# Kernel tuning notes

Measured on AMD Instinct MI355X. Metric: run time of the kernel, lower is better.

Reference implementation:

```python
import jax, jax.numpy as jnp
import numpy as np

N = 100000
E = 3200000
D = 128


def setup_inputs() -> dict:
    key = jax.random.key(0)
    k1, k2, k3, k4 = jax.random.split(key, 4)
    x = jax.random.normal(k1, (N, D), dtype=jnp.float32)
    edge_index = jax.random.randint(k2, (2, E), 0, N, dtype=jnp.int64)
    W1 = jax.random.normal(k3, (D, 16), dtype=jnp.float32) * (1.0 / np.sqrt(D))
    b1 = jnp.zeros((16,), dtype=jnp.float32)
    W2 = jax.random.normal(k4, (16, 2), dtype=jnp.float32) * (1.0 / np.sqrt(16))
    b2 = jnp.zeros((2,), dtype=jnp.float32)
    return {"x": x, "edge_index": edge_index, "W1": W1, "b1": b1, "W2": W2, "b2": b2}


def _gcn_conv(h, src, dst, norm, W, b):
    # transform first (out_dim <= in_dim), then normalized scatter-add aggregation
    h = h @ W                                   # [N, out]
    msg = h[src] * norm[:, None]                # [E+N, out] gathered messages
    agg = jax.ops.segment_sum(msg, dst, num_segments=N)
    return agg + b


def reference(x, edge_index, W1, b1, W2, b2):
    loops = jnp.arange(N, dtype=edge_index.dtype)
    src = jnp.concatenate([edge_index[0], loops])   # row (message source)
    dst = jnp.concatenate([edge_index[1], loops])   # col (aggregation target)
    # symmetric GCN normalization: deg over dst, norm = d^-1/2[src] * d^-1/2[dst]
    deg = jax.ops.segment_sum(jnp.ones_like(src, dtype=x.dtype), dst, num_segments=N)
    dinv = jnp.where(deg > 0, jax.lax.rsqrt(deg), 0.0)
    norm = dinv[src] * dinv[dst]

    h = _gcn_conv(x, src, dst, norm, W1, b1)
    h = jax.nn.relu(h)
    h = _gcn_conv(h, src, dst, norm, W2, b2)
    return jax.nn.log_softmax(h, axis=1)
```

## Files before the change

### kernel.cpp

```cpp
#include <hip/hip_runtime.h>
#include <hip/hip_fp16.h>
#include <math.h>

#define N_NODES 100000
#define N_EDGES 3200000
#define D_IN    128
#define H1      16

#define PSH     8
#define NPB     200
#define NB      500
#define CAP     9936
#define PBLK    512
#define CHUNK   6250
#define ELS_CAP 13760
#define NLINES  (ELS_CAP / 16)
#define MROWS   64

__device__ __forceinline__ unsigned bkt(int d) {
    return (unsigned)(((unsigned long long)(unsigned)d * 671089ull) >> 27);
}


__global__ __launch_bounds__(512) void k_partition(const int* __restrict__ ei,
                                                   int* __restrict__ cursor,
                                                   unsigned int* __restrict__ eop) {
    __shared__ int h[512];
    __shared__ int loff[512];
    __shared__ int resv[NB];
    __shared__ int wsum[8], wpre[8];
    __shared__ unsigned short owner[NLINES];
    __shared__ unsigned char rank8[CHUNK];
    __shared__ unsigned int els[ELS_CAP];
    int t = threadIdx.x;
    h[t] = 0;
    __syncthreads();
    int c0 = blockIdx.x * CHUNK;
    const int2* s2 = (const int2*)(ei + c0);
    const int2* d2 = (const int2*)(ei + N_EDGES + c0);
    for (int i = t; i < CHUNK / 2; i += 512) {
        int2 dd = d2[i];
        rank8[2 * i]     = (unsigned char)atomicAdd(&h[bkt(dd.x)], 1);
        rank8[2 * i + 1] = (unsigned char)atomicAdd(&h[bkt(dd.y)], 1);
    }
    __syncthreads();
    int cp = (h[t] + 15) & ~15;
    int lane = t & 63, w = t >> 6;
    int v = cp;
#pragma unroll
    for (int o = 1; o < 64; o <<= 1) {
        int u = __shfl_up(v, o);
        if (lane >= o) v += u;
    }
    if (lane == 63) wsum[w] = v;
    __syncthreads();
    if (t < 8) {
        int s = wsum[t];
#pragma unroll
        for (int o = 1; o < 8; o <<= 1) {
            int u = __shfl_up(s, o);
            if (t >= o) s += u;
        }
        wpre[t] = s;
    }
    __syncthreads();
    int inc = v + ((w > 0) ? wpre[w - 1] : 0);
    int totalpad = wpre[7];
    int ex = inc - cp;
    loff[t] = ex;
    if (t < NB && cp) {
        resv[t] = atomicAdd(&cursor[t], cp);
        int l0 = ex >> 4;
        for (int k = 0; k < (cp >> 4); ++k) owner[l0 + k] = (unsigned short)t;
    }
    for (int i = t; i < totalpad; i += 512) els[i] = 0xFFFFFFFFu;
    __syncthreads();
    for (int i = t; i < CHUNK / 2; i += 512) {
        int2 ss = s2[i];
        int2 dd = d2[i];
        unsigned bx = bkt(dd.x), by = bkt(dd.y);
        els[loff[bx] + (int)rank8[2 * i]] =
            ((unsigned)ss.x << PSH) | (unsigned)(dd.x - (int)(bx * NPB));
        els[loff[by] + (int)rank8[2 * i + 1]] =
            ((unsigned)ss.y << PSH) | (unsigned)(dd.y - (int)(by * NPB));
    }
    __syncthreads();
    for (int i = t; i < totalpad; i += 512) {
        int b   = owner[i >> 4];
        int pos = resv[b] + (i - loff[b]);
        if (pos < CAP)
            eop[(size_t)b * CAP + pos] = els[i];
    }
}

__global__ __launch_bounds__(512) void k_build(const int* __restrict__ cursor,
                                               unsigned int* __restrict__ eop,
                                               int* __restrict__ nstart,
                                               int* __restrict__ ndeg,
                                               float* __restrict__ dinv) {
    __shared__ unsigned int els[CAP];
    __shared__ int cnt[256];
    __shared__ int off[256];
    __shared__ int wsum[4], wpre[4];
    int t = threadIdx.x, b = blockIdx.x;
    if (t < 256) cnt[t] = 0;
    __syncthreads();
    int n = cursor[b]; if (n > CAP) n = CAP;
    unsigned int* reg = eop + (size_t)b * CAP;
    for (int i4 = t; i4 < (n >> 2); i4 += 512) {
        uint4 wv = ((const uint4*)reg)[i4];
        unsigned int e0 = wv.x, e1 = wv.y, e2 = wv.z, e3 = wv.w;
        int r;
        if ((int)e0 >= 0) { r = atomicAdd(&cnt[e0 & 0xFF], 1); e0 |= (unsigned)r << 25; }
        if ((int)e1 >= 0) { r = atomicAdd(&cnt[e1 & 0xFF], 1); e1 |= (unsigned)r << 25; }
        if ((int)e2 >= 0) { r = atomicAdd(&cnt[e2 & 0xFF], 1); e2 |= (unsigned)r << 25; }
        if ((int)e3 >= 0) { r = atomicAdd(&cnt[e3 & 0xFF], 1); e3 |= (unsigned)r << 25; }
        ((uint4*)els)[i4] = make_uint4(e0, e1, e2, e3);
    }
    __syncthreads();
    int lane = t & 63, w = t >> 6;
    int v = 0;
    if (t < 256) {
        v = cnt[t];
#pragma unroll
        for (int o = 1; o < 64; o <<= 1) {
            int u = __shfl_up(v, o);
            if (lane >= o) v += u;
        }
        if (lane == 63) wsum[w] = v;
    }
    __syncthreads();
    if (t < 4) {
        int s = wsum[t];
#pragma unroll
        for (int o = 1; o < 4; o <<= 1) {
            int u = __shfl_up(s, o);
            if (t >= o) s += u;
        }
        wpre[t] = s;
    }
    __syncthreads();
    if (t < 256) {
        int val = cnt[t];
        int ex = (v + ((w > 0) ? wpre[w - 1] : 0)) - val;
        off[t] = ex;
        if (t < NPB) {
            int node = b * NPB + t;
            nstart[node] = b * CAP + ex;
            ndeg[node]   = val;
            dinv[node]   = rsqrtf((float)(val + 1));
        }
    }
    __syncthreads();
    for (int i4 = t; i4 < (n >> 2); i4 += 512) {
        uint4 wv = ((const uint4*)els)[i4];
        unsigned int e; unsigned s;
        e = wv.x; s = (e >> PSH) & 0x1FFFFu;
        if (s < N_NODES) reg[off[e & 0xFF] + (int)(e >> 25)] = s;
        e = wv.y; s = (e >> PSH) & 0x1FFFFu;
        if (s < N_NODES) reg[off[e & 0xFF] + (int)(e >> 25)] = s;
        e = wv.z; s = (e >> PSH) & 0x1FFFFu;
        if (s < N_NODES) reg[off[e & 0xFF] + (int)(e >> 25)] = s;
        e = wv.w; s = (e >> PSH) & 0x1FFFFu;
        if (s < N_NODES) reg[off[e & 0xFF] + (int)(e >> 25)] = s;
    }
}

__global__ __launch_bounds__(256) void k_mm1(const float* __restrict__ x,
                                             const float* __restrict__ W1,
                                             const float* __restrict__ dinv,
                                             __half* __restrict__ h1h) {
    __shared__ float sX[MROWS][D_IN + 1];
    int t = threadIdx.x;
    int r0 = blockIdx.x * MROWS;
    for (int i = t; i < MROWS * (D_IN / 4); i += 256) {
        int row = i >> 5, c4 = i & 31;
        int grow = r0 + row;
        float4 v = (grow < N_NODES) ? ((const float4*)x)[(size_t)grow * 32 + c4]
                                    : make_float4(0.f, 0.f, 0.f, 0.f);
        sX[row][c4 * 4 + 0] = v.x; sX[row][c4 * 4 + 1] = v.y;
        sX[row][c4 * 4 + 2] = v.z; sX[row][c4 * 4 + 3] = v.w;
    }
    __syncthreads();
    int lane = t & 63;
    int c0 = __builtin_amdgcn_readfirstlane((t >> 6) * 4);
    float a0 = 0.f, a1 = 0.f, a2 = 0.f, a3 = 0.f;
#pragma unroll 4
    for (int d = 0; d < D_IN; ++d) {
        float xv = sX[lane][d];
        a0 = fmaf(xv, W1[d * 16 + c0 + 0], a0);
        a1 = fmaf(xv, W1[d * 16 + c0 + 1], a1);
        a2 = fmaf(xv, W1[d * 16 + c0 + 2], a2);
        a3 = fmaf(xv, W1[d * 16 + c0 + 3], a3);
    }
    int grow = r0 + lane;
    if (grow < N_NODES) {
        float di = dinv[grow];
        __half2* o = (__half2*)(h1h + (size_t)grow * H1 + c0);
        o[0] = __floats2half2_rn(a0 * di, a1 * di);
        o[1] = __floats2half2_rn(a2 * di, a3 * di);
    }
}

__global__ __launch_bounds__(256) void k_agg1(const unsigned int* __restrict__ eop,
                                              const int* __restrict__ nstart,
                                              const int* __restrict__ ndeg,
                                              const __half* __restrict__ h1h,
                                              const float* __restrict__ dinv,
                                              const float* __restrict__ b1,
                                              const float* __restrict__ W2,
                                              float2* __restrict__ h2f) {
    int t = threadIdx.x;
    int g = t >> 3, l = t & 7;
    int base = (t & 63) & ~7;
    int node = blockIdx.x * 32 + g;
    int e0 = nstart[node], deg = ndeg[node];
    const __half2* H = (const __half2*)h1h;
    float a0 = 0.f, a1 = 0.f, c0 = 0.f, c1 = 0.f;
    int nfull = deg & ~7;
    int j = e0;
    for (; j < e0 + nfull; j += 8) {
        int s = (int)eop[j + l];
#pragma unroll
        for (int k = 0; k < 8; k += 2) {
            int sk0 = __shfl(s, base + k);
            int sk1 = __shfl(s, base + k + 1);
            float2 f0 = __half22float2(H[sk0 * 8 + l]);
            float2 f1 = __half22float2(H[sk1 * 8 + l]);
            a0 += f0.x; a1 += f0.y;
            c0 += f1.x; c1 += f1.y;
        }
    }
    int r = e0 + deg - j;
    if (r) {
        int s = (l < r) ? (int)eop[j + l] : -1;
#pragma unroll
        for (int k = 0; k < 8; ++k) {
            int sk = __shfl(s, base + k);
            int su = (sk >= 0) ? sk : 0;
            float m = (sk >= 0) ? 1.f : 0.f;
            float2 f = __half22float2(H[su * 8 + l]);
            a0 = fmaf(f.x, m, a0); a1 = fmaf(f.y, m, a1);
        }
    }
    float di = dinv[node];
    float2 self = __half22float2(H[node * 8 + l]);
    float s0 = (a0 + c0) + self.x, s1 = (a1 + c1) + self.y;
    float2 bb = ((const float2*)b1)[l];
    float h0 = fmaxf(fmaf(di, s0, bb.x), 0.f);
    float h1v = fmaxf(fmaf(di, s1, bb.y), 0.f);
    float4 wv = ((const float4*)W2)[l];
    float p0 = h0 * wv.x + h1v * wv.z;
    float p1 = h0 * wv.y + h1v * wv.w;
#pragma unroll
    for (int off = 1; off < 8; off <<= 1) {
        p0 += __shfl_xor(p0, off);
        p1 += __shfl_xor(p1, off);
    }
    if (l == 0) h2f[node] = make_float2(p0 * di, p1 * di);
}

__global__ __launch_bounds__(256) void k_agg2(const unsigned int* __restrict__ eop,
                                              const int* __restrict__ nstart,
                                              const int* __restrict__ ndeg,
                                              const float2* __restrict__ h2f,
                                              const float* __restrict__ dinv,
                                              const float* __restrict__ b2,
                                              float* __restrict__ out) {
    int tg = blockIdx.x * 256 + threadIdx.x;
    int node = tg >> 2, l = tg & 3;
    if (node >= N_NODES) return;
    int e0 = nstart[node], e1 = e0 + ndeg[node];
    float ax = 0.f, ay = 0.f;
    for (int j = e0 + l; j < e1; j += 4) {
        float2 m = h2f[eop[j]];
        ax += m.x; ay += m.y;
    }
    ax += __shfl_xor(ax, 1); ay += __shfl_xor(ay, 1);
    ax += __shfl_xor(ax, 2); ay += __shfl_xor(ay, 2);
    if (l == 0) {
        float di = dinv[node];
        float2 self = h2f[node];
        float a0 = fmaf(di, ax + self.x, b2[0]);
        float a1 = fmaf(di, ay + self.y, b2[1]);
        float m  = fmaxf(a0, a1);
        float lg = logf(expf(a0 - m) + expf(a1 - m));
        out[2 * node]     = a0 - m - lg;
        out[2 * node + 1] = a1 - m - lg;
    }
}

extern "C" void kernel_launch(void* const* d_in, const int* in_sizes, int n_in,
                              void* d_out, int out_size, void* d_ws, size_t ws_size,
                              hipStream_t stream) {
    const float* x  = (const float*)d_in[0];
    const int*   ei = (const int*)d_in[1];
    const float* W1 = (const float*)d_in[2];
    const float* b1 = (const float*)d_in[3];
    const float* W2 = (const float*)d_in[4];
    const float* b2 = (const float*)d_in[5];
    float* out = (float*)d_out;

    int*          cursor = (int*)d_ws;
    int*          nstart = cursor + 512;
    int*          ndeg   = nstart + 100352;
    float*        dinv   = (float*)(ndeg + 100352);
    __half*       h1h    = (__half*)(dinv + 100352);
    float2*       h2f    = (float2*)(h1h + (size_t)100352 * H1);
    unsigned int* eop    = (unsigned int*)(h2f + 100352);

    hipMemsetAsync(cursor, 0, 512 * sizeof(int), stream);
    k_partition<<<PBLK, 512, 0, stream>>>(ei, cursor, eop);
    k_build    <<<NB,   512, 0, stream>>>(cursor, eop, nstart, ndeg, dinv);
    k_mm1      <<<(N_NODES + MROWS - 1) / MROWS, 256, 0, stream>>>(x, W1, dinv, h1h);
    k_agg1     <<<N_NODES / 32, 256, 0, stream>>>(eop, nstart, ndeg, h1h, dinv, b1, W2, h2f);
    k_agg2     <<<(N_NODES * 4 + 255) / 256, 256, 0, stream>>>(eop, nstart, ndeg, h2f, dinv, b2, out);
}
```

Baseline: 204.0 us.

## Pad cursor atomics, vectorize partition stores, register-stage build, prefetch edge indices

Several independent tweaks land together. The per-bucket cursors are spread 32 ints apart to avoid atomic contention on shared cache lines, and partition fill/flush now uses uint4 vector stores. The build kernel keeps its tagged edges in registers (up to 5 uint4 per thread) instead of a large LDS array, which frees shared memory for occupancy. The agg1 and agg2 kernels software-prefetch the next batch of edge indices, and agg2 moves from 4 to 8 lanes per node. The register staging in build assumes n/4 <= 5*512, and CAP satisfies that.

```diff
diff --git a/kernel.cpp b/kernel.cpp
--- a/kernel.cpp
+++ b/kernel.cpp
@@ -15,7 +15,9 @@
 #define CHUNK   6250
 #define ELS_CAP 13760
 #define NLINES  (ELS_CAP / 16)
+#define CSTRIDE 32
 #define MROWS   64
+#define BITQ    5
 
 __device__ __forceinline__ unsigned bkt(int d) {
     return (unsigned)(((unsigned long long)(unsigned)d * 671089ull) >> 27);
@@ -69,11 +71,12 @@
     int ex = inc - cp;
     loff[t] = ex;
     if (t < NB && cp) {
-        resv[t] = atomicAdd(&cursor[t], cp);
+        resv[t] = atomicAdd(&cursor[t * CSTRIDE], cp);
         int l0 = ex >> 4;
         for (int k = 0; k < (cp >> 4); ++k) owner[l0 + k] = (unsigned short)t;
     }
-    for (int i = t; i < totalpad; i += 512) els[i] = 0xFFFFFFFFu;
+    for (int i4 = t; i4 < (totalpad >> 2); i4 += 512)
+        ((uint4*)els)[i4] = make_uint4(0xFFFFFFFFu, 0xFFFFFFFFu, 0xFFFFFFFFu, 0xFFFFFFFFu);
     __syncthreads();
     for (int i = t; i < CHUNK / 2; i += 512) {
         int2 ss = s2[i];
@@ -85,11 +88,11 @@
             ((unsigned)ss.y << PSH) | (unsigned)(dd.y - (int)(by * NPB));
     }
     __syncthreads();
-    for (int i = t; i < totalpad; i += 512) {
-        int b   = owner[i >> 4];
-        int pos = resv[b] + (i - loff[b]);
-        if (pos < CAP)
-            eop[(size_t)b * CAP + pos] = els[i];
+    for (int i4 = t; i4 < (totalpad >> 2); i4 += 512) {
+        int b   = owner[i4 >> 2];
+        int pos = resv[b] + (4 * i4 - loff[b]);
+        if (pos + 3 < CAP)
+            *(uint4*)(eop + (size_t)b * CAP + pos) = ((const uint4*)els)[i4];
     }
 }
 
@@ -98,24 +101,29 @@
                                                int* __restrict__ nstart,
                                                int* __restrict__ ndeg,
                                                float* __restrict__ dinv) {
-    __shared__ unsigned int els[CAP];
     __shared__ int cnt[256];
     __shared__ int off[256];
     __shared__ int wsum[4], wpre[4];
     int t = threadIdx.x, b = blockIdx.x;
     if (t < 256) cnt[t] = 0;
     __syncthreads();
-    int n = cursor[b]; if (n > CAP) n = CAP;
+    int n = cursor[b * CSTRIDE]; if (n > CAP) n = CAP;
+    int nq = n >> 2;
     unsigned int* reg = eop + (size_t)b * CAP;
-    for (int i4 = t; i4 < (n >> 2); i4 += 512) {
-        uint4 wv = ((const uint4*)reg)[i4];
-        unsigned int e0 = wv.x, e1 = wv.y, e2 = wv.z, e3 = wv.w;
-        int r;
-        if ((int)e0 >= 0) { r = atomicAdd(&cnt[e0 & 0xFF], 1); e0 |= (unsigned)r << 25; }
-        if ((int)e1 >= 0) { r = atomicAdd(&cnt[e1 & 0xFF], 1); e1 |= (unsigned)r << 25; }
-        if ((int)e2 >= 0) { r = atomicAdd(&cnt[e2 & 0xFF], 1); e2 |= (unsigned)r << 25; }
-        if ((int)e3 >= 0) { r = atomicAdd(&cnt[e3 & 0xFF], 1); e3 |= (unsigned)r << 25; }
-        ((uint4*)els)[i4] = make_uint4(e0, e1, e2, e3);
+    uint4 st[BITQ];
+#pragma unroll
+    for (int it = 0; it < BITQ; ++it) {
+        int i4 = t + it * 512;
+        if (i4 < nq) {
+            uint4 wv = ((const uint4*)reg)[i4];
+            unsigned int e0 = wv.x, e1 = wv.y, e2 = wv.z, e3 = wv.w;
+            int r;
+            if ((int)e0 >= 0) { r = atomicAdd(&cnt[e0 & 0xFF], 1); e0 |= (unsigned)r << 25; }
+            if ((int)e1 >= 0) { r = atomicAdd(&cnt[e1 & 0xFF], 1); e1 |= (unsigned)r << 25; }
+            if ((int)e2 >= 0) { r = atomicAdd(&cnt[e2 & 0xFF], 1); e2 |= (unsigned)r << 25; }
+            if ((int)e3 >= 0) { r = atomicAdd(&cnt[e3 & 0xFF], 1); e3 |= (unsigned)r << 25; }
+            st[it] = make_uint4(e0, e1, e2, e3);
+        }
     }
     __syncthreads();
     int lane = t & 63, w = t >> 6;
@@ -152,17 +160,21 @@
         }
     }
     __syncthreads();
-    for (int i4 = t; i4 < (n >> 2); i4 += 512) {
-        uint4 wv = ((const uint4*)els)[i4];
-        unsigned int e; unsigned s;
-        e = wv.x; s = (e >> PSH) & 0x1FFFFu;
-        if (s < N_NODES) reg[off[e & 0xFF] + (int)(e >> 25)] = s;
-        e = wv.y; s = (e >> PSH) & 0x1FFFFu;
-        if (s < N_NODES) reg[off[e & 0xFF] + (int)(e >> 25)] = s;
-        e = wv.z; s = (e >> PSH) & 0x1FFFFu;
-        if (s < N_NODES) reg[off[e & 0xFF] + (int)(e >> 25)] = s;
-        e = wv.w; s = (e >> PSH) & 0x1FFFFu;
-        if (s < N_NODES) reg[off[e & 0xFF] + (int)(e >> 25)] = s;
+#pragma unroll
+    for (int it = 0; it < BITQ; ++it) {
+        int i4 = t + it * 512;
+        if (i4 < nq) {
+            uint4 wv = st[it];
+            unsigned int e; unsigned s;
+            e = wv.x; s = (e >> PSH) & 0x1FFFFu;
+            if (s < N_NODES) reg[off[e & 0xFF] + (int)((e >> 25) & 0x7F)] = s;
+            e = wv.y; s = (e >> PSH) & 0x1FFFFu;
+            if (s < N_NODES) reg[off[e & 0xFF] + (int)((e >> 25) & 0x7F)] = s;
+            e = wv.z; s = (e >> PSH) & 0x1FFFFu;
+            if (s < N_NODES) reg[off[e & 0xFF] + (int)((e >> 25) & 0x7F)] = s;
+            e = wv.w; s = (e >> PSH) & 0x1FFFFu;
+            if (s < N_NODES) reg[off[e & 0xFF] + (int)((e >> 25) & 0x7F)] = s;
+        }
     }
 }
 
@@ -218,22 +230,24 @@
     const __half2* H = (const __half2*)h1h;
     float a0 = 0.f, a1 = 0.f, c0 = 0.f, c1 = 0.f;
     int nfull = deg & ~7;
-    int j = e0;
-    for (; j < e0 + nfull; j += 8) {
-        int s = (int)eop[j + l];
+    int jend = e0 + nfull;
+    int s_cur = (nfull > 0) ? (int)eop[e0 + l] : 0;
+    for (int j = e0; j < jend; j += 8) {
+        int s_nxt = (j + 8 < jend) ? (int)eop[j + 8 + l] : 0;
 #pragma unroll
         for (int k = 0; k < 8; k += 2) {
-            int sk0 = __shfl(s, base + k);
-            int sk1 = __shfl(s, base + k + 1);
+            int sk0 = __shfl(s_cur, base + k);
+            int sk1 = __shfl(s_cur, base + k + 1);
             float2 f0 = __half22float2(H[sk0 * 8 + l]);
             float2 f1 = __half22float2(H[sk1 * 8 + l]);
             a0 += f0.x; a1 += f0.y;
             c0 += f1.x; c1 += f1.y;
         }
-    }
-    int r = e0 + deg - j;
+        s_cur = s_nxt;
+    }
+    int r = deg - nfull;
     if (r) {
-        int s = (l < r) ? (int)eop[j + l] : -1;
+        int s = (l < r) ? (int)eop[jend + l] : -1;
 #pragma unroll
         for (int k = 0; k < 8; ++k) {
             int sk = __shfl(s, base + k);
@@ -268,16 +282,20 @@
                                               const float* __restrict__ b2,
                                               float* __restrict__ out) {
     int tg = blockIdx.x * 256 + threadIdx.x;
-    int node = tg >> 2, l = tg & 3;
-    if (node >= N_NODES) return;
+    int node = tg >> 3, l = tg & 7;
     int e0 = nstart[node], e1 = e0 + ndeg[node];
     float ax = 0.f, ay = 0.f;
-    for (int j = e0 + l; j < e1; j += 4) {
-        float2 m = h2f[eop[j]];
+    int j = e0 + l;
+    int sj = (j < e1) ? (int)eop[j] : 0;
+    for (; j < e1; j += 8) {
+        int sn = (j + 8 < e1) ? (int)eop[j + 8] : 0;
+        float2 m = h2f[sj];
         ax += m.x; ay += m.y;
+        sj = sn;
     }
     ax += __shfl_xor(ax, 1); ay += __shfl_xor(ay, 1);
     ax += __shfl_xor(ax, 2); ay += __shfl_xor(ay, 2);
+    ax += __shfl_xor(ax, 4); ay += __shfl_xor(ay, 4);
     if (l == 0) {
         float di = dinv[node];
         float2 self = h2f[node];
@@ -302,17 +320,18 @@
     float* out = (float*)d_out;
 
     int*          cursor = (int*)d_ws;
-    int*          nstart = cursor + 512;
+    int*          nstart = cursor + 16384;
     int*          ndeg   = nstart + 100352;
     float*        dinv   = (float*)(ndeg + 100352);
     __half*       h1h    = (__half*)(dinv + 100352);
     float2*       h2f    = (float2*)(h1h + (size_t)100352 * H1);
     unsigned int* eop    = (unsigned int*)(h2f + 100352);
 
-    hipMemsetAsync(cursor, 0, 512 * sizeof(int), stream);
+    hipMemsetAsync(cursor, 0, 16384 * sizeof(int), stream);
+
     k_partition<<<PBLK, 512, 0, stream>>>(ei, cursor, eop);
     k_build    <<<NB,   512, 0, stream>>>(cursor, eop, nstart, ndeg, dinv);
     k_mm1      <<<(N_NODES + MROWS - 1) / MROWS, 256, 0, stream>>>(x, W1, dinv, h1h);
     k_agg1     <<<N_NODES / 32, 256, 0, stream>>>(eop, nstart, ndeg, h1h, dinv, b1, W2, h2f);
-    k_agg2     <<<(N_NODES * 4 + 255) / 256, 256, 0, stream>>>(eop, nstart, ndeg, h2f, dinv, b2, out);
-}
+    k_agg2     <<<N_NODES / 32, 256, 0, stream>>>(eop, nstart, ndeg, h2f, dinv, b2, out);
+}
```

After: 199.9 us. 1.02x faster.
